# Kernel tuning notes

Measured on AMD Instinct MI355X. Metric: run time of the kernel, lower is better.

## Reference

```python
import jax, jax.numpy as jnp
import numpy as np

N = 100_000      # nodes
E = 1_600_000    # edges (avg degree 16)
D_IN, D_H, D_OUT = 128, 128, 64


def setup_inputs() -> dict:
    key = jax.random.key(0)
    ks = jax.random.split(key, 6)
    x = jax.random.normal(ks[0], (N, D_IN), jnp.float32)
    edge_index = jax.random.randint(ks[1], (2, E), 0, N, dtype=jnp.int32)
    W1 = jax.random.normal(ks[2], (D_IN, D_H), jnp.float32) / np.sqrt(D_IN)
    b1 = jnp.zeros((D_H,), jnp.float32)
    W2 = jax.random.normal(ks[3], (D_H, D_OUT), jnp.float32) / np.sqrt(D_H)
    b2 = jnp.zeros((D_OUT,), jnp.float32)
    return {"x": x, "edge_index": edge_index, "W1": W1, "b1": b1, "W2": W2, "b2": b2}


def _gcn_layer(x, W, b, src, dst, n_nodes):
    # PyG GCNConv: h = x @ W; symmetric norm with self-loops; scatter-add; + bias
    h = x @ W                                        # [N, D_out]
    deg = jax.ops.segment_sum(jnp.ones_like(dst, jnp.float32), dst,
                              num_segments=n_nodes)  # self-loops => deg >= 1
    dinv = jax.lax.rsqrt(deg)                        # deg^{-1/2}
    norm = dinv[src] * dinv[dst]                     # [E+N]
    msg = h[src] * norm[:, None]                     # gather + scale
    out = jax.ops.segment_sum(msg, dst, num_segments=n_nodes)  # scatter-add
    return out + b


def reference(x, edge_index, W1, b1, W2, b2):
    n = x.shape[0]
    loop = jnp.arange(n, dtype=edge_index.dtype)
    src = jnp.concatenate([edge_index[0], loop])     # add self-loops
    dst = jnp.concatenate([edge_index[1], loop])
    h = _gcn_layer(x, W1, b1, src, dst, n)
    h = jax.nn.relu(h)
    # dropout(p=0.5) is identity in eval mode
    out = _gcn_layer(h, W2, b2, src, dst, n)
    return out
```

## Files before the change

### kernel.cpp

```cpp
#include <hip/hip_runtime.h>
#include <hip/hip_bf16.h>


#define NTHREADS 256
#define BSH 8
#define NBMAX 512
#define BCAP 5632
#define FC_CAP 8192

typedef unsigned int uint;
typedef unsigned short ushort;
typedef __attribute__((ext_vector_type(8))) short short8;
typedef __attribute__((ext_vector_type(4))) float floatx4;

__device__ __forceinline__ uint pack_bf16(float a, float b) {
    __hip_bfloat162 h = __float22bfloat162_rn(make_float2(a, b));
    return *reinterpret_cast<uint*>(&h);
}
__device__ __forceinline__ float bf16_lo(uint q) { return __uint_as_float(q << 16); }
__device__ __forceinline__ float bf16_hi(uint q) { return __uint_as_float(q & 0xffff0000u); }

__global__ __launch_bounds__(256) void partition_kernel(
    const int* __restrict__ src, const int* __restrict__ dst,
    int* __restrict__ bfill, uint* __restrict__ staged, int e, int nb) {
    __shared__ uint eP[2048];
    __shared__ ushort eB[2048];
    __shared__ int hist[NBMAX];
    __shared__ int base[NBMAX];
    int t = threadIdx.x;
    int e0 = blockIdx.x * 2048;

    for (int b = t; b < nb; b += 256) hist[b] = 0;
    __syncthreads();
#pragma unroll
    for (int v = 0; v < 2; v++) {
        int li = t * 8 + v * 4;
        int gi = e0 + li;
        int4 s4, d4;
        if (gi + 3 < e) {
            s4 = *(const int4*)&src[gi];
            d4 = *(const int4*)&dst[gi];
        } else {
            const int* sp = &src[gi];
            const int* dp = &dst[gi];
            s4.x = (gi + 0 < e) ? sp[0] : 0;  d4.x = (gi + 0 < e) ? dp[0] : -1;
            s4.y = (gi + 1 < e) ? sp[1] : 0;  d4.y = (gi + 1 < e) ? dp[1] : -1;
            s4.z = (gi + 2 < e) ? sp[2] : 0;  d4.z = (gi + 2 < e) ? dp[2] : -1;
            s4.w = (gi + 3 < e) ? sp[3] : 0;  d4.w = (gi + 3 < e) ? dp[3] : -1;
        }
        uint4 p4;
        p4.x = ((uint)s4.x << 8) | ((uint)d4.x & 255u);
        p4.y = ((uint)s4.y << 8) | ((uint)d4.y & 255u);
        p4.z = ((uint)s4.z << 8) | ((uint)d4.z & 255u);
        p4.w = ((uint)s4.w << 8) | ((uint)d4.w & 255u);
        *(uint4*)&eP[li] = p4;
        eB[li + 0] = (d4.x >= 0) ? (ushort)(d4.x >> BSH) : (ushort)0xFFFF;
        eB[li + 1] = (d4.y >= 0) ? (ushort)(d4.y >> BSH) : (ushort)0xFFFF;
        eB[li + 2] = (d4.z >= 0) ? (ushort)(d4.z >> BSH) : (ushort)0xFFFF;
        eB[li + 3] = (d4.w >= 0) ? (ushort)(d4.w >> BSH) : (ushort)0xFFFF;
        if (d4.x >= 0) atomicAdd(&hist[d4.x >> BSH], 1);
        if (d4.y >= 0) atomicAdd(&hist[d4.y >> BSH], 1);
        if (d4.z >= 0) atomicAdd(&hist[d4.z >> BSH], 1);
        if (d4.w >= 0) atomicAdd(&hist[d4.w >> BSH], 1);
    }
    __syncthreads();
    for (int b = t; b < nb; b += 256) {
        int v = hist[b];
        base[b] = v ? (b * BCAP + atomicAdd(&bfill[b], v)) : 0;
        hist[b] = 0;
    }
    __syncthreads();
#pragma unroll
    for (int i = 0; i < 8; i++) {
        int li = t + i * 256;
        ushort bb = eB[li];
        if (bb != (ushort)0xFFFF) {
            int r = atomicAdd(&hist[bb], 1);
            staged[base[bb] + r] = eP[li];
        }
    }
}

__global__ __launch_bounds__(256) void fine_csr_kernel(
    const uint* __restrict__ staged, const int* __restrict__ bfill,
    int4* __restrict__ meta, float* __restrict__ dinv,
    int* __restrict__ rec, int n) {
    __shared__ uint eL[FC_CAP];
    __shared__ int lcnt[256];
    __shared__ int tsum[256];
    __shared__ int red[256];
    int b = blockIdx.x;
    int t = threadIdx.x;

    int part = 0;
    for (int j = t; j < b; j += 256) part += bfill[j];
    red[t] = part;
    lcnt[t] = 0;
    __syncthreads();
    for (int off = 128; off > 0; off >>= 1) {
        if (t < off) red[t] += red[t + off];
        __syncthreads();
    }
    int s0 = red[0];
    int m = bfill[b];

    int sb = b * BCAP;
    for (int i = t; i < m; i += 256) {
        uint pk = staged[sb + i];
        eL[i] = pk;
        atomicAdd(&lcnt[pk & 255u], 1);
    }
    __syncthreads();
    int v = lcnt[t];
    tsum[t] = v;
    __syncthreads();
    int x = v;
    for (int off = 1; off < 256; off <<= 1) {
        int y = (t >= off) ? tsum[t - off] : 0;
        __syncthreads();
        x += y;
        tsum[t] = x;
        __syncthreads();
    }
    int excl = x - v;
    int node = (b << BSH) + t;
    if (node < n) {
        float di = rsqrtf((float)v + 1.0f);
        dinv[node] = di;
        meta[node] = make_int4(s0 + excl, v, __float_as_int(di), __float_as_int(di * di));
    }
    lcnt[t] = s0 + excl;
    __syncthreads();
    for (int i = t; i < m; i += 256) {
        uint pk = eL[i];
        int pos = atomicAdd(&lcnt[pk & 255u], 1);
        rec[pos] = (int)(pk >> 8);
    }
}

template <int COLS, bool XF32>
__global__ __launch_bounds__(256) void gemm_mfma(const void* __restrict__ Xv,
                                                 const float* __restrict__ W,
                                                 uint* __restrict__ Cq,
                                                 const float* __restrict__ dscale,
                                                 int n) {
    __shared__ ushort sX[64 * 128];
    __shared__ ushort sWT[COLS * 128];
    int t = threadIdx.x;
    int rbase = blockIdx.x * 64;

    if (XF32) {
        const float* X = (const float*)Xv;
#pragma unroll
        for (int i = 0; i < 8; i++) {
            int f = t + 256 * i;
            int r = f >> 5;
            int c4 = f & 31;
            float4 v = make_float4(0.f, 0.f, 0.f, 0.f);
            int gr = rbase + r;
            if (gr < n) v = *(const float4*)(X + (size_t)gr * 128 + c4 * 4);
            uint lo = pack_bf16(v.x, v.y);
            uint hi = pack_bf16(v.z, v.w);
            int chunk = c4 >> 1;
            int sub = (c4 & 1) * 4;
            int off = r * 128 + (((chunk ^ (r & 15)) << 3) + sub);
            *(uint2*)&sX[off] = make_uint2(lo, hi);
        }
    } else {
        const ushort* X = (const ushort*)Xv;
#pragma unroll
        for (int i = 0; i < 4; i++) {
            int f = t + 256 * i;
            int r = f >> 4;
            int chunk = f & 15;
            uint4 v = make_uint4(0, 0, 0, 0);
            int gr = rbase + r;
            if (gr < n) v = *(const uint4*)(X + (size_t)gr * 128 + chunk * 8);
            int off = r * 128 + ((chunk ^ (r & 15)) << 3);
            *(uint4*)&sX[off] = v;
        }
    }
    {
        constexpr int UNITS = 64 * (COLS / 4);
        constexpr int PER_T = UNITS / 256;
#pragma unroll
        for (int i = 0; i < PER_T; i++) {
            int u = t + 256 * i;
            int kp = u / (COLS / 4);
            int n4 = u % (COLS / 4);
            int k = kp * 2;
            float4 w0 = *(const float4*)(W + (size_t)k * COLS + n4 * 4);
            float4 w1 = *(const float4*)(W + (size_t)(k + 1) * COLS + n4 * 4);
            int chunk = k >> 3;
            int sub = k & 7;
            const float* a0 = (const float*)&w0;
            const float* a1 = (const float*)&w1;
#pragma unroll
            for (int j = 0; j < 4; j++) {
                int nn = n4 * 4 + j;
                uint pk = pack_bf16(a0[j], a1[j]);
                int off = nn * 128 + (((chunk ^ (nn & 15)) << 3) + sub);
                *(uint*)&sWT[off] = pk;
            }
        }
    }
    __syncthreads();

    int lane = t & 63;
    int wave = t >> 6;
    int m = lane & 15;
    int q = lane >> 4;
    int r0 = wave * 16;

    floatx4 acc[COLS / 16];
#pragma unroll
    for (int c = 0; c < COLS / 16; c++) acc[c] = (floatx4){0.f, 0.f, 0.f, 0.f};

#pragma unroll
    for (int ks = 0; ks < 4; ks++) {
        int rr = r0 + m;
        int ca = (ks * 4 + q) ^ (rr & 15);
        short8 afrag = *(const short8*)&sX[rr * 128 + (ca << 3)];
#pragma unroll
        for (int c = 0; c < COLS / 16; c++) {
            int nn = c * 16 + m;
            int cb = (ks * 4 + q) ^ (nn & 15);
            short8 bfrag = *(const short8*)&sWT[nn * 128 + (cb << 3)];
            acc[c] = __builtin_amdgcn_mfma_f32_16x16x32_bf16(bfrag, afrag, acc[c], 0, 0, 0);
        }
    }

    int gr = rbase + r0 + m;
    if (gr < n) {
        float sc = dscale[gr];
#pragma unroll
        for (int c = 0; c < COLS / 16; c++) {
            uint2 pk;
            pk.x = pack_bf16(acc[c][0] * sc, acc[c][1] * sc);
            pk.y = pack_bf16(acc[c][2] * sc, acc[c][3] * sc);
            *(uint2*)&Cq[(size_t)gr * (COLS / 2) + c * 8 + q * 2] = pk;
        }
    }
}

__global__ __launch_bounds__(512) void agg128_mm64(
    const uint* __restrict__ hq, const int* __restrict__ rec,
    const int4* __restrict__ meta, const float* __restrict__ dinv,
    const float* __restrict__ bias, const float* __restrict__ W2,
    uint* __restrict__ h2q, int n) {
    __shared__ ushort sWT[64 * 128];
    __shared__ ushort sg[32 * 128];
    int t = threadIdx.x;

#pragma unroll
    for (int i = 0; i < 2; i++) {
        int u = t + 512 * i;
        int kp = u >> 4;
        int n4 = u & 15;
        int k = kp * 2;
        float4 w0 = *(const float4*)(W2 + (size_t)k * 64 + n4 * 4);
        float4 w1 = *(const float4*)(W2 + (size_t)(k + 1) * 64 + n4 * 4);
        int chunk = k >> 3;
        int sub = k & 7;
        const float* a0f = (const float*)&w0;
        const float* a1f = (const float*)&w1;
#pragma unroll
        for (int j = 0; j < 4; j++) {
            int nn = n4 * 4 + j;
            uint pk = pack_bf16(a0f[j], a1f[j]);
            *(uint*)&sWT[nn * 128 + (((chunk ^ (nn & 15)) << 3) + sub)] = pk;
        }
    }

    int qw = t >> 4;
    int fl = t & 15;
    int nb0 = blockIdx.x * 32;
    int w = nb0 + qw;
    bool valid = w < n;
    int wsafe = valid ? w : 0;
    const uint4* h4 = (const uint4*)hq;

    int4 mt = meta[wsafe];
    int j0 = mt.x;
    int deg = valid ? mt.y : 0;
    float di = __int_as_float(mt.z);

    uint4 qs = h4[(size_t)wsafe * 16 + fl];
    float a0 = bf16_lo(qs.x), a1 = bf16_hi(qs.x);
    float a2 = bf16_lo(qs.y), a3 = bf16_hi(qs.y);
    float a4 = bf16_lo(qs.z), a5 = bf16_hi(qs.z);
    float a6 = bf16_lo(qs.w), a7 = bf16_hi(qs.w);
    if (!valid) { a0 = a1 = a2 = a3 = a4 = a5 = a6 = a7 = 0.f; }

    const int* rp = rec + j0;
    int tt = 0;
    for (; tt + 8 <= deg; tt += 8) {
        int s[8]; uint4 q[8];
#pragma unroll
        for (int u = 0; u < 8; u++) s[u] = rp[tt + u];
#pragma unroll
        for (int u = 0; u < 8; u++) q[u] = h4[(size_t)s[u] * 16 + fl];
#pragma unroll
        for (int u = 0; u < 8; u++) {
            a0 += bf16_lo(q[u].x); a1 += bf16_hi(q[u].x);
            a2 += bf16_lo(q[u].y); a3 += bf16_hi(q[u].y);
            a4 += bf16_lo(q[u].z); a5 += bf16_hi(q[u].z);
            a6 += bf16_lo(q[u].w); a7 += bf16_hi(q[u].w);
        }
    }
    for (; tt + 2 <= deg; tt += 2) {
        int s0i = rp[tt], s1i = rp[tt + 1];
        uint4 q0 = h4[(size_t)s0i * 16 + fl];
        uint4 q1 = h4[(size_t)s1i * 16 + fl];
        a0 += bf16_lo(q0.x) + bf16_lo(q1.x);
        a1 += bf16_hi(q0.x) + bf16_hi(q1.x);
        a2 += bf16_lo(q0.y) + bf16_lo(q1.y);
        a3 += bf16_hi(q0.y) + bf16_hi(q1.y);
        a4 += bf16_lo(q0.z) + bf16_lo(q1.z);
        a5 += bf16_hi(q0.z) + bf16_hi(q1.z);
        a6 += bf16_lo(q0.w) + bf16_lo(q1.w);
        a7 += bf16_hi(q0.w) + bf16_hi(q1.w);
    }
    if (tt < deg) {
        int s = rp[tt];
        uint4 q0 = h4[(size_t)s * 16 + fl];
        a0 += bf16_lo(q0.x); a1 += bf16_hi(q0.x);
        a2 += bf16_lo(q0.y); a3 += bf16_hi(q0.y);
        a4 += bf16_lo(q0.z); a5 += bf16_hi(q0.z);
        a6 += bf16_lo(q0.w); a7 += bf16_hi(q0.w);
    }

    float4 bb0 = *(const float4*)&bias[8 * fl];
    float4 bb1 = *(const float4*)&bias[8 * fl + 4];
    uint4 pkv;
    pkv.x = pack_bf16(fmaxf(di * a0 + bb0.x, 0.f), fmaxf(di * a1 + bb0.y, 0.f));
    pkv.y = pack_bf16(fmaxf(di * a2 + bb0.z, 0.f), fmaxf(di * a3 + bb0.w, 0.f));
    pkv.z = pack_bf16(fmaxf(di * a4 + bb1.x, 0.f), fmaxf(di * a5 + bb1.y, 0.f));
    pkv.w = pack_bf16(fmaxf(di * a6 + bb1.z, 0.f), fmaxf(di * a7 + bb1.w, 0.f));
    *(uint4*)&sg[qw * 128 + ((fl ^ (qw & 15)) << 3)] = pkv;
    __syncthreads();

    int wave = t >> 6;
    int lane = t & 63;
    int m = lane & 15;
    int qq = lane >> 4;
    int rt = wave >> 2;
    int ct = wave & 3;
    floatx4 acc = (floatx4){0.f, 0.f, 0.f, 0.f};
#pragma unroll
    for (int ks = 0; ks < 4; ks++) {
        int rr = rt * 16 + m;
        int ca = (ks * 4 + qq) ^ (rr & 15);
        short8 afrag = *(const short8*)&sg[rr * 128 + (ca << 3)];
        int nn = ct * 16 + m;
        int cb = (ks * 4 + qq) ^ (nn & 15);
        short8 bfrag = *(const short8*)&sWT[nn * 128 + (cb << 3)];
        acc = __builtin_amdgcn_mfma_f32_16x16x32_bf16(bfrag, afrag, acc, 0, 0, 0);
    }
    int gr = nb0 + rt * 16 + m;
    if (gr < n) {
        float sc = dinv[gr];
        uint2 pk;
        pk.x = pack_bf16(acc[0] * sc, acc[1] * sc);
        pk.y = pack_bf16(acc[2] * sc, acc[3] * sc);
        *(uint2*)&h2q[(size_t)gr * 32 + ct * 8 + qq * 2] = pk;
    }
}

__global__ __launch_bounds__(256) void aggregate64q(
    const uint* __restrict__ hq, const int* __restrict__ rec,
    const int4* __restrict__ meta, const float* __restrict__ bias,
    float* __restrict__ out, int n) {
    int gt = blockIdx.x * 256 + threadIdx.x;
    int w = gt >> 3;
    if (w >= n) return;
    int fl = gt & 7;

    int4 mt = meta[w];
    int j0 = mt.x;
    int deg = mt.y;
    float di = __int_as_float(mt.z);
    const uint4* h4 = (const uint4*)hq;

    uint4 qs = h4[(size_t)w * 8 + fl];
    float a0 = bf16_lo(qs.x), a1 = bf16_hi(qs.x);
    float a2 = bf16_lo(qs.y), a3 = bf16_hi(qs.y);
    float a4 = bf16_lo(qs.z), a5 = bf16_hi(qs.z);
    float a6 = bf16_lo(qs.w), a7 = bf16_hi(qs.w);

    const int* rp = rec + j0;
    int tt = 0;
    for (; tt + 8 <= deg; tt += 8) {
        int s[8]; uint4 q[8];
#pragma unroll
        for (int u = 0; u < 8; u++) s[u] = rp[tt + u];
#pragma unroll
        for (int u = 0; u < 8; u++) q[u] = h4[(size_t)s[u] * 8 + fl];
#pragma unroll
        for (int u = 0; u < 8; u++) {
            a0 += bf16_lo(q[u].x); a1 += bf16_hi(q[u].x);
            a2 += bf16_lo(q[u].y); a3 += bf16_hi(q[u].y);
            a4 += bf16_lo(q[u].z); a5 += bf16_hi(q[u].z);
            a6 += bf16_lo(q[u].w); a7 += bf16_hi(q[u].w);
        }
    }
    for (; tt + 2 <= deg; tt += 2) {
        int s0i = rp[tt], s1i = rp[tt + 1];
        uint4 q0 = h4[(size_t)s0i * 8 + fl];
        uint4 q1 = h4[(size_t)s1i * 8 + fl];
        a0 += bf16_lo(q0.x) + bf16_lo(q1.x);
        a1 += bf16_hi(q0.x) + bf16_hi(q1.x);
        a2 += bf16_lo(q0.y) + bf16_lo(q1.y);
        a3 += bf16_hi(q0.y) + bf16_hi(q1.y);
        a4 += bf16_lo(q0.z) + bf16_lo(q1.z);
        a5 += bf16_hi(q0.z) + bf16_hi(q1.z);
        a6 += bf16_lo(q0.w) + bf16_lo(q1.w);
        a7 += bf16_hi(q0.w) + bf16_hi(q1.w);
    }
    if (tt < deg) {
        int s = rp[tt];
        uint4 q0 = h4[(size_t)s * 8 + fl];
        a0 += bf16_lo(q0.x); a1 += bf16_hi(q0.x);
        a2 += bf16_lo(q0.y); a3 += bf16_hi(q0.y);
        a4 += bf16_lo(q0.z); a5 += bf16_hi(q0.z);
        a6 += bf16_lo(q0.w); a7 += bf16_hi(q0.w);
    }

    float4 bb0 = *(const float4*)&bias[8 * fl];
    float4 bb1 = *(const float4*)&bias[8 * fl + 4];
    float4 o0, o1;
    o0.x = di * a0 + bb0.x; o0.y = di * a1 + bb0.y;
    o0.z = di * a2 + bb0.z; o0.w = di * a3 + bb0.w;
    o1.x = di * a4 + bb1.x; o1.y = di * a5 + bb1.y;
    o1.z = di * a6 + bb1.z; o1.w = di * a7 + bb1.w;
    *(float4*)&out[(size_t)w * 64 + 8 * fl] = o0;
    *(float4*)&out[(size_t)w * 64 + 8 * fl + 4] = o1;
}

extern "C" void kernel_launch(void* const* d_in, const int* in_sizes, int n_in,
                              void* d_out, int out_size, void* d_ws, size_t ws_size,
                              hipStream_t stream) {
    const float* x = (const float*)d_in[0];
    const int* edge = (const int*)d_in[1];
    const float* W1 = (const float*)d_in[2];
    const float* b1 = (const float*)d_in[3];
    const float* W2 = (const float*)d_in[4];
    const float* b2 = (const float*)d_in[5];

    const int N = in_sizes[0] / 128;
    const int E = in_sizes[1] / 2;
    const int* src = edge;
    const int* dst = edge + E;
    const int NB = (N + (1 << BSH) - 1) >> BSH;

    char* p = (char*)d_ws;
    int* bfill = (int*)p;     p += NBMAX * 4;
    float* dinv = (float*)p;  p += (size_t)N * 4;
    int4* meta = (int4*)p;    p += (size_t)N * 16;
    int* rec = (int*)p;       p += (size_t)E * 4;
    uint* staged = (uint*)p;  p += (size_t)NBMAX * BCAP * 4;
    uint* hq = (uint*)p;      p += (size_t)N * 64 * 4;
    uint* h2q = (uint*)p;     p += (size_t)N * 32 * 4;

    float* out = (float*)d_out;
    const int eblocks = (E + 2047) / 2048;

    (void)hipMemsetAsync(bfill, 0, NBMAX * 4, stream);
    partition_kernel<<<eblocks, 256, 0, stream>>>(src, dst, bfill, staged, E, NB);
    fine_csr_kernel<<<NB, 256, 0, stream>>>(staged, bfill, meta, dinv, rec, N);

    const int gblocks = (N + 63) / 64;

    gemm_mfma<128, true><<<gblocks, 256, 0, stream>>>(x, W1, hq, dinv, N);
    agg128_mm64<<<(N + 31) / 32, 512, 0, stream>>>(hq, rec, meta, dinv, b1, W2, h2q, N);
    aggregate64q<<<(N * 8 + 255) / 256, 256, 0, stream>>>(h2q, rec, meta, b2, out, N);
}
```

Measured before the change: 274.9 us.

## Merge edge partitioning and first GEMM into one launch, move dinv scaling to aggregation

The first layer's GEMM no longer pre-scales rows by dinv, so it no longer depends on the degree computation. It is merged into the same launch as the edge partition kernel, with block ranges selecting which role each block runs. The first aggregation now applies a per-edge weight dinv[src]*dinv[dst] and a self-loop weight from meta. This removes one launch and lets partition and GEMM overlap. In exchange it adds an extra gather of dinv per edge and one multiply per feature in the aggregation inner loop, and raises shared memory per block to 48KB for the partition blocks.

```diff
diff --git a/kernel.cpp b/kernel.cpp
--- a/kernel.cpp
+++ b/kernel.cpp
@@ -20,137 +20,75 @@
 __device__ __forceinline__ float bf16_lo(uint q) { return __uint_as_float(q << 16); }
 __device__ __forceinline__ float bf16_hi(uint q) { return __uint_as_float(q & 0xffff0000u); }
 
-__global__ __launch_bounds__(256) void partition_kernel(
+__global__ __launch_bounds__(256) void part_gemm1(
     const int* __restrict__ src, const int* __restrict__ dst,
-    int* __restrict__ bfill, uint* __restrict__ staged, int e, int nb) {
-    __shared__ uint eP[2048];
-    __shared__ ushort eB[2048];
-    __shared__ int hist[NBMAX];
-    __shared__ int base[NBMAX];
+    int* __restrict__ bfill, uint* __restrict__ staged, int e, int nb, int eblocks,
+    const float* __restrict__ X, const float* __restrict__ W1,
+    uint* __restrict__ hq, int n) {
+    __shared__ __align__(16) char smem[49152];
     int t = threadIdx.x;
-    int e0 = blockIdx.x * 2048;
-
-    for (int b = t; b < nb; b += 256) hist[b] = 0;
-    __syncthreads();
-#pragma unroll
-    for (int v = 0; v < 2; v++) {
-        int li = t * 8 + v * 4;
-        int gi = e0 + li;
-        int4 s4, d4;
-        if (gi + 3 < e) {
-            s4 = *(const int4*)&src[gi];
-            d4 = *(const int4*)&dst[gi];
-        } else {
-            const int* sp = &src[gi];
-            const int* dp = &dst[gi];
-            s4.x = (gi + 0 < e) ? sp[0] : 0;  d4.x = (gi + 0 < e) ? dp[0] : -1;
-            s4.y = (gi + 1 < e) ? sp[1] : 0;  d4.y = (gi + 1 < e) ? dp[1] : -1;
-            s4.z = (gi + 2 < e) ? sp[2] : 0;  d4.z = (gi + 2 < e) ? dp[2] : -1;
-            s4.w = (gi + 3 < e) ? sp[3] : 0;  d4.w = (gi + 3 < e) ? dp[3] : -1;
-        }
-        uint4 p4;
-        p4.x = ((uint)s4.x << 8) | ((uint)d4.x & 255u);
-        p4.y = ((uint)s4.y << 8) | ((uint)d4.y & 255u);
-        p4.z = ((uint)s4.z << 8) | ((uint)d4.z & 255u);
-        p4.w = ((uint)s4.w << 8) | ((uint)d4.w & 255u);
-        *(uint4*)&eP[li] = p4;
-        eB[li + 0] = (d4.x >= 0) ? (ushort)(d4.x >> BSH) : (ushort)0xFFFF;
-        eB[li + 1] = (d4.y >= 0) ? (ushort)(d4.y >> BSH) : (ushort)0xFFFF;
-        eB[li + 2] = (d4.z >= 0) ? (ushort)(d4.z >> BSH) : (ushort)0xFFFF;
-        eB[li + 3] = (d4.w >= 0) ? (ushort)(d4.w >> BSH) : (ushort)0xFFFF;
-        if (d4.x >= 0) atomicAdd(&hist[d4.x >> BSH], 1);
-        if (d4.y >= 0) atomicAdd(&hist[d4.y >> BSH], 1);
-        if (d4.z >= 0) atomicAdd(&hist[d4.z >> BSH], 1);
-        if (d4.w >= 0) atomicAdd(&hist[d4.w >> BSH], 1);
-    }
-    __syncthreads();
-    for (int b = t; b < nb; b += 256) {
-        int v = hist[b];
-        base[b] = v ? (b * BCAP + atomicAdd(&bfill[b], v)) : 0;
-        hist[b] = 0;
-    }
-    __syncthreads();
-#pragma unroll
-    for (int i = 0; i < 8; i++) {
-        int li = t + i * 256;
-        ushort bb = eB[li];
-        if (bb != (ushort)0xFFFF) {
-            int r = atomicAdd(&hist[bb], 1);
-            staged[base[bb] + r] = eP[li];
-        }
-    }
-}
-
-__global__ __launch_bounds__(256) void fine_csr_kernel(
-    const uint* __restrict__ staged, const int* __restrict__ bfill,
-    int4* __restrict__ meta, float* __restrict__ dinv,
-    int* __restrict__ rec, int n) {
-    __shared__ uint eL[FC_CAP];
-    __shared__ int lcnt[256];
-    __shared__ int tsum[256];
-    __shared__ int red[256];
-    int b = blockIdx.x;
-    int t = threadIdx.x;
-
-    int part = 0;
-    for (int j = t; j < b; j += 256) part += bfill[j];
-    red[t] = part;
-    lcnt[t] = 0;
-    __syncthreads();
-    for (int off = 128; off > 0; off >>= 1) {
-        if (t < off) red[t] += red[t + off];
-        __syncthreads();
-    }
-    int s0 = red[0];
-    int m = bfill[b];
-
-    int sb = b * BCAP;
-    for (int i = t; i < m; i += 256) {
-        uint pk = staged[sb + i];
-        eL[i] = pk;
-        atomicAdd(&lcnt[pk & 255u], 1);
-    }
-    __syncthreads();
-    int v = lcnt[t];
-    tsum[t] = v;
-    __syncthreads();
-    int x = v;
-    for (int off = 1; off < 256; off <<= 1) {
-        int y = (t >= off) ? tsum[t - off] : 0;
-        __syncthreads();
-        x += y;
-        tsum[t] = x;
-        __syncthreads();
-    }
-    int excl = x - v;
-    int node = (b << BSH) + t;
-    if (node < n) {
-        float di = rsqrtf((float)v + 1.0f);
-        dinv[node] = di;
-        meta[node] = make_int4(s0 + excl, v, __float_as_int(di), __float_as_int(di * di));
-    }
-    lcnt[t] = s0 + excl;
-    __syncthreads();
-    for (int i = t; i < m; i += 256) {
-        uint pk = eL[i];
-        int pos = atomicAdd(&lcnt[pk & 255u], 1);
-        rec[pos] = (int)(pk >> 8);
-    }
-}
-
-template <int COLS, bool XF32>
-__global__ __launch_bounds__(256) void gemm_mfma(const void* __restrict__ Xv,
-                                                 const float* __restrict__ W,
-                                                 uint* __restrict__ Cq,
-                                                 const float* __restrict__ dscale,
-                                                 int n) {
-    __shared__ ushort sX[64 * 128];
-    __shared__ ushort sWT[COLS * 128];
-    int t = threadIdx.x;
-    int rbase = blockIdx.x * 64;
-
-    if (XF32) {
-        const float* X = (const float*)Xv;
+
+    if ((int)blockIdx.x < eblocks) {
+        uint* eP = (uint*)smem;
+        ushort* eB = (ushort*)(smem + 8192);
+        int* hist = (int*)(smem + 12288);
+        int* base = (int*)(smem + 14336);
+        int e0 = blockIdx.x * 2048;
+
+        for (int b = t; b < nb; b += 256) hist[b] = 0;
+        __syncthreads();
+#pragma unroll
+        for (int v = 0; v < 2; v++) {
+            int li = t * 8 + v * 4;
+            int gi = e0 + li;
+            int4 s4, d4;
+            if (gi + 3 < e) {
+                s4 = *(const int4*)&src[gi];
+                d4 = *(const int4*)&dst[gi];
+            } else {
+                const int* sp = &src[gi];
+                const int* dp = &dst[gi];
+                s4.x = (gi + 0 < e) ? sp[0] : 0;  d4.x = (gi + 0 < e) ? dp[0] : -1;
+                s4.y = (gi + 1 < e) ? sp[1] : 0;  d4.y = (gi + 1 < e) ? dp[1] : -1;
+                s4.z = (gi + 2 < e) ? sp[2] : 0;  d4.z = (gi + 2 < e) ? dp[2] : -1;
+                s4.w = (gi + 3 < e) ? sp[3] : 0;  d4.w = (gi + 3 < e) ? dp[3] : -1;
+            }
+            uint4 p4;
+            p4.x = ((uint)s4.x << 8) | ((uint)d4.x & 255u);
+            p4.y = ((uint)s4.y << 8) | ((uint)d4.y & 255u);
+            p4.z = ((uint)s4.z << 8) | ((uint)d4.z & 255u);
+            p4.w = ((uint)s4.w << 8) | ((uint)d4.w & 255u);
+            *(uint4*)&eP[li] = p4;
+            eB[li + 0] = (d4.x >= 0) ? (ushort)(d4.x >> BSH) : (ushort)0xFFFF;
+            eB[li + 1] = (d4.y >= 0) ? (ushort)(d4.y >> BSH) : (ushort)0xFFFF;
+            eB[li + 2] = (d4.z >= 0) ? (ushort)(d4.z >> BSH) : (ushort)0xFFFF;
+            eB[li + 3] = (d4.w >= 0) ? (ushort)(d4.w >> BSH) : (ushort)0xFFFF;
+            if (d4.x >= 0) atomicAdd(&hist[d4.x >> BSH], 1);
+            if (d4.y >= 0) atomicAdd(&hist[d4.y >> BSH], 1);
+            if (d4.z >= 0) atomicAdd(&hist[d4.z >> BSH], 1);
+            if (d4.w >= 0) atomicAdd(&hist[d4.w >> BSH], 1);
+        }
+        __syncthreads();
+        for (int b = t; b < nb; b += 256) {
+            int v = hist[b];
+            base[b] = v ? (b * BCAP + atomicAdd(&bfill[b], v)) : 0;
+            hist[b] = 0;
+        }
+        __syncthreads();
+#pragma unroll
+        for (int i = 0; i < 8; i++) {
+            int li = t + i * 256;
+            ushort bb = eB[li];
+            if (bb != (ushort)0xFFFF) {
+                int r = atomicAdd(&hist[bb], 1);
+                staged[base[bb] + r] = eP[li];
+            }
+        }
+    } else {
+        ushort* sX = (ushort*)smem;
+        ushort* sWT = (ushort*)(smem + 16384);
+        int rbase = ((int)blockIdx.x - eblocks) * 64;
+
 #pragma unroll
         for (int i = 0; i < 8; i++) {
             int f = t + 256 * i;
@@ -166,31 +104,14 @@
             int off = r * 128 + (((chunk ^ (r & 15)) << 3) + sub);
             *(uint2*)&sX[off] = make_uint2(lo, hi);
         }
-    } else {
-        const ushort* X = (const ushort*)Xv;
-#pragma unroll
-        for (int i = 0; i < 4; i++) {
-            int f = t + 256 * i;
-            int r = f >> 4;
-            int chunk = f & 15;
-            uint4 v = make_uint4(0, 0, 0, 0);
-            int gr = rbase + r;
-            if (gr < n) v = *(const uint4*)(X + (size_t)gr * 128 + chunk * 8);
-            int off = r * 128 + ((chunk ^ (r & 15)) << 3);
-            *(uint4*)&sX[off] = v;
-        }
-    }
-    {
-        constexpr int UNITS = 64 * (COLS / 4);
-        constexpr int PER_T = UNITS / 256;
-#pragma unroll
-        for (int i = 0; i < PER_T; i++) {
+#pragma unroll
+        for (int i = 0; i < 8; i++) {
             int u = t + 256 * i;
-            int kp = u / (COLS / 4);
-            int n4 = u % (COLS / 4);
+            int kp = u >> 5;
+            int n4 = u & 31;
             int k = kp * 2;
-            float4 w0 = *(const float4*)(W + (size_t)k * COLS + n4 * 4);
-            float4 w1 = *(const float4*)(W + (size_t)(k + 1) * COLS + n4 * 4);
+            float4 w0 = *(const float4*)(W1 + (size_t)k * 128 + n4 * 4);
+            float4 w1 = *(const float4*)(W1 + (size_t)(k + 1) * 128 + n4 * 4);
             int chunk = k >> 3;
             int sub = k & 7;
             const float* a0 = (const float*)&w0;
@@ -203,43 +124,99 @@
                 *(uint*)&sWT[off] = pk;
             }
         }
-    }
+        __syncthreads();
+
+        int lane = t & 63;
+        int wave = t >> 6;
+        int m = lane & 15;
+        int q = lane >> 4;
+        int r0 = wave * 16;
+
+        floatx4 acc[8];
+#pragma unroll
+        for (int c = 0; c < 8; c++) acc[c] = (floatx4){0.f, 0.f, 0.f, 0.f};
+
+#pragma unroll
+        for (int ks = 0; ks < 4; ks++) {
+            int rr = r0 + m;
+            int ca = (ks * 4 + q) ^ (rr & 15);
+            short8 afrag = *(const short8*)&sX[rr * 128 + (ca << 3)];
+#pragma unroll
+            for (int c = 0; c < 8; c++) {
+                int nn = c * 16 + m;
+                int cb = (ks * 4 + q) ^ (nn & 15);
+                short8 bfrag = *(const short8*)&sWT[nn * 128 + (cb << 3)];
+                acc[c] = __builtin_amdgcn_mfma_f32_16x16x32_bf16(bfrag, afrag, acc[c], 0, 0, 0);
+            }
+        }
+
+        int gr = rbase + r0 + m;
+        if (gr < n) {
+#pragma unroll
+            for (int c = 0; c < 8; c++) {
+                uint2 pk;
+                pk.x = pack_bf16(acc[c][0], acc[c][1]);
+                pk.y = pack_bf16(acc[c][2], acc[c][3]);
+                *(uint2*)&hq[(size_t)gr * 64 + c * 8 + q * 2] = pk;
+            }
+        }
+    }
+}
+
+__global__ __launch_bounds__(256) void fine_csr_kernel(
+    const uint* __restrict__ staged, const int* __restrict__ bfill,
+    int4* __restrict__ meta, float* __restrict__ dinv,
+    int* __restrict__ rec, int n) {
+    __shared__ uint eL[FC_CAP];
+    __shared__ int lcnt[256];
+    __shared__ int tsum[256];
+    __shared__ int red[256];
+    int b = blockIdx.x;
+    int t = threadIdx.x;
+
+    int part = 0;
+    for (int j = t; j < b; j += 256) part += bfill[j];
+    red[t] = part;
+    lcnt[t] = 0;
     __syncthreads();
-
-    int lane = t & 63;
-    int wave = t >> 6;
-    int m = lane & 15;
-    int q = lane >> 4;
-    int r0 = wave * 16;
-
-    floatx4 acc[COLS / 16];
-#pragma unroll
-    for (int c = 0; c < COLS / 16; c++) acc[c] = (floatx4){0.f, 0.f, 0.f, 0.f};
-
-#pragma unroll
-    for (int ks = 0; ks < 4; ks++) {
-        int rr = r0 + m;
-        int ca = (ks * 4 + q) ^ (rr & 15);
-        short8 afrag = *(const short8*)&sX[rr * 128 + (ca << 3)];
-#pragma unroll
-        for (int c = 0; c < COLS / 16; c++) {
-            int nn = c * 16 + m;
-            int cb = (ks * 4 + q) ^ (nn & 15);
-            short8 bfrag = *(const short8*)&sWT[nn * 128 + (cb << 3)];
-            acc[c] = __builtin_amdgcn_mfma_f32_16x16x32_bf16(bfrag, afrag, acc[c], 0, 0, 0);
-        }
-    }
-
-    int gr = rbase + r0 + m;
-    if (gr < n) {
-        float sc = dscale[gr];
-#pragma unroll
-        for (int c = 0; c < COLS / 16; c++) {
-            uint2 pk;
-            pk.x = pack_bf16(acc[c][0] * sc, acc[c][1] * sc);
-            pk.y = pack_bf16(acc[c][2] * sc, acc[c][3] * sc);
-            *(uint2*)&Cq[(size_t)gr * (COLS / 2) + c * 8 + q * 2] = pk;
-        }
+    for (int off = 128; off > 0; off >>= 1) {
+        if (t < off) red[t] += red[t + off];
+        __syncthreads();
+    }
+    int s0 = red[0];
+    int m = bfill[b];
+
+    int sb = b * BCAP;
+    for (int i = t; i < m; i += 256) {
+        uint pk = staged[sb + i];
+        eL[i] = pk;
+        atomicAdd(&lcnt[pk & 255u], 1);
+    }
+    __syncthreads();
+    int v = lcnt[t];
+    tsum[t] = v;
+    __syncthreads();
+    int x = v;
+    for (int off = 1; off < 256; off <<= 1) {
+        int y = (t >= off) ? tsum[t - off] : 0;
+        __syncthreads();
+        x += y;
+        tsum[t] = x;
+        __syncthreads();
+    }
+    int excl = x - v;
+    int node = (b << BSH) + t;
+    if (node < n) {
+        float di = rsqrtf((float)v + 1.0f);
+        dinv[node] = di;
+        meta[node] = make_int4(s0 + excl, v, __float_as_int(di), __float_as_int(di * di));
+    }
+    lcnt[t] = s0 + excl;
+    __syncthreads();
+    for (int i = t; i < m; i += 256) {
+        uint pk = eL[i];
+        int pos = atomicAdd(&lcnt[pk & 255u], 1);
+        rec[pos] = (int)(pk >> 8);
     }
 }
 
@@ -284,59 +261,63 @@
     int j0 = mt.x;
     int deg = valid ? mt.y : 0;
     float di = __int_as_float(mt.z);
+    float swq = valid ? __int_as_float(mt.w) : 0.f;
 
     uint4 qs = h4[(size_t)wsafe * 16 + fl];
-    float a0 = bf16_lo(qs.x), a1 = bf16_hi(qs.x);
-    float a2 = bf16_lo(qs.y), a3 = bf16_hi(qs.y);
-    float a4 = bf16_lo(qs.z), a5 = bf16_hi(qs.z);
-    float a6 = bf16_lo(qs.w), a7 = bf16_hi(qs.w);
-    if (!valid) { a0 = a1 = a2 = a3 = a4 = a5 = a6 = a7 = 0.f; }
+    float a0 = bf16_lo(qs.x) * swq, a1 = bf16_hi(qs.x) * swq;
+    float a2 = bf16_lo(qs.y) * swq, a3 = bf16_hi(qs.y) * swq;
+    float a4 = bf16_lo(qs.z) * swq, a5 = bf16_hi(qs.z) * swq;
+    float a6 = bf16_lo(qs.w) * swq, a7 = bf16_hi(qs.w) * swq;
 
     const int* rp = rec + j0;
     int tt = 0;
     for (; tt + 8 <= deg; tt += 8) {
-        int s[8]; uint4 q[8];
+        int s[8]; float wf[8]; uint4 q[8];
 #pragma unroll
         for (int u = 0; u < 8; u++) s[u] = rp[tt + u];
 #pragma unroll
+        for (int u = 0; u < 8; u++) wf[u] = dinv[s[u]] * di;
+#pragma unroll
         for (int u = 0; u < 8; u++) q[u] = h4[(size_t)s[u] * 16 + fl];
 #pragma unroll
         for (int u = 0; u < 8; u++) {
-            a0 += bf16_lo(q[u].x); a1 += bf16_hi(q[u].x);
-            a2 += bf16_lo(q[u].y); a3 += bf16_hi(q[u].y);
-            a4 += bf16_lo(q[u].z); a5 += bf16_hi(q[u].z);
-            a6 += bf16_lo(q[u].w); a7 += bf16_hi(q[u].w);
+            a0 += bf16_lo(q[u].x) * wf[u]; a1 += bf16_hi(q[u].x) * wf[u];
+            a2 += bf16_lo(q[u].y) * wf[u]; a3 += bf16_hi(q[u].y) * wf[u];
+            a4 += bf16_lo(q[u].z) * wf[u]; a5 += bf16_hi(q[u].z) * wf[u];
+            a6 += bf16_lo(q[u].w) * wf[u]; a7 += bf16_hi(q[u].w) * wf[u];
         }
     }
     for (; tt + 2 <= deg; tt += 2) {
         int s0i = rp[tt], s1i = rp[tt + 1];
+        float w0v = dinv[s0i] * di, w1v = dinv[s1i] * di;
         uint4 q0 = h4[(size_t)s0i * 16 + fl];
         uint4 q1 = h4[(size_t)s1i * 16 + fl];
-        a0 += bf16_lo(q0.x) + bf16_lo(q1.x);
-        a1 += bf16_hi(q0.x) + bf16_hi(q1.x);
-        a2 += bf16_lo(q0.y) + bf16_lo(q1.y);
-        a3 += bf16_hi(q0.y) + bf16_hi(q1.y);
-        a4 += bf16_lo(q0.z) + bf16_lo(q1.z);
-        a5 += bf16_hi(q0.z) + bf16_hi(q1.z);
-        a6 += bf16_lo(q0.w) + bf16_lo(q1.w);
-        a7 += bf16_hi(q0.w) + bf16_hi(q1.w);
+        a0 += bf16_lo(q0.x) * w0v + bf16_lo(q1.x) * w1v;
+        a1 += bf16_hi(q0.x) * w0v + bf16_hi(q1.x) * w1v;
+        a2 += bf16_lo(q0.y) * w0v + bf16_lo(q1.y) * w1v;
+        a3 += bf16_hi(q0.y) * w0v + bf16_hi(q1.y) * w1v;
+        a4 += bf16_lo(q0.z) * w0v + bf16_lo(q1.z) * w1v;
+        a5 += bf16_hi(q0.z) * w0v + bf16_hi(q1.z) * w1v;
+        a6 += bf16_lo(q0.w) * w0v + bf16_lo(q1.w) * w1v;
+        a7 += bf16_hi(q0.w) * w0v + bf16_hi(q1.w) * w1v;
     }
     if (tt < deg) {
         int s = rp[tt];
+        float wv = dinv[s] * di;
         uint4 q0 = h4[(size_t)s * 16 + fl];
-        a0 += bf16_lo(q0.x); a1 += bf16_hi(q0.x);
-        a2 += bf16_lo(q0.y); a3 += bf16_hi(q0.y);
-        a4 += bf16_lo(q0.z); a5 += bf16_hi(q0.z);
-        a6 += bf16_lo(q0.w); a7 += bf16_hi(q0.w);
+        a0 += bf16_lo(q0.x) * wv; a1 += bf16_hi(q0.x) * wv;
+        a2 += bf16_lo(q0.y) * wv; a3 += bf16_hi(q0.y) * wv;
+        a4 += bf16_lo(q0.z) * wv; a5 += bf16_hi(q0.z) * wv;
+        a6 += bf16_lo(q0.w) * wv; a7 += bf16_hi(q0.w) * wv;
     }
 
     float4 bb0 = *(const float4*)&bias[8 * fl];
     float4 bb1 = *(const float4*)&bias[8 * fl + 4];
     uint4 pkv;
-    pkv.x = pack_bf16(fmaxf(di * a0 + bb0.x, 0.f), fmaxf(di * a1 + bb0.y, 0.f));
-    pkv.y = pack_bf16(fmaxf(di * a2 + bb0.z, 0.f), fmaxf(di * a3 + bb0.w, 0.f));
-    pkv.z = pack_bf16(fmaxf(di * a4 + bb1.x, 0.f), fmaxf(di * a5 + bb1.y, 0.f));
-    pkv.w = pack_bf16(fmaxf(di * a6 + bb1.z, 0.f), fmaxf(di * a7 + bb1.w, 0.f));
+    pkv.x = pack_bf16(fmaxf(a0 + bb0.x, 0.f), fmaxf(a1 + bb0.y, 0.f));
+    pkv.y = pack_bf16(fmaxf(a2 + bb0.z, 0.f), fmaxf(a3 + bb0.w, 0.f));
+    pkv.z = pack_bf16(fmaxf(a4 + bb1.x, 0.f), fmaxf(a5 + bb1.y, 0.f));
+    pkv.w = pack_bf16(fmaxf(a6 + bb1.z, 0.f), fmaxf(a7 + bb1.w, 0.f));
     *(uint4*)&sg[qw * 128 + ((fl ^ (qw & 15)) << 3)] = pkv;
     __syncthreads();
 
@@ -464,14 +445,12 @@
 
     float* out = (float*)d_out;
     const int eblocks = (E + 2047) / 2048;
+    const int gblocks = (N + 63) / 64;
 
     (void)hipMemsetAsync(bfill, 0, NBMAX * 4, stream);
-    partition_kernel<<<eblocks, 256, 0, stream>>>(src, dst, bfill, staged, E, NB);
+    part_gemm1<<<eblocks + gblocks, 256, 0, stream>>>(
+        src, dst, bfill, staged, E, NB, eblocks, x, W1, hq, N);
     fine_csr_kernel<<<NB, 256, 0, stream>>>(staged, bfill, meta, dinv, rec, N);
-
-    const int gblocks = (N + 63) / 64;
-
-    gemm_mfma<128, true><<<gblocks, 256, 0, stream>>>(x, W1, hq, dinv, N);
     agg128_mm64<<<(N + 31) / 32, 512, 0, stream>>>(hq, rec, meta, dinv, b1, W2, h2q, N);
     aggregate64q<<<(N * 8 + 255) / 256, 256, 0, stream>>>(h2q, rec, meta, b2, out, N);
 }
```

Measured after the change: 267.9 us. 2.5% less time.
